# Kernel tuning notes

Measured on AMD Instinct MI355X. Metric: run time of the kernel, lower is better.

The kernel has to match this reference:

```python
import jax, jax.numpy as jnp
import numpy as np

N_CLASSES = 10   # number of distinct private-attribute labels
DIM = 16         # PCA / GMM dimension (init arg `dim`)
SIGMA = 1.0      # init arg `sigma`, cov = sigma * I


def _pca(X, k):
    # torch PCA: center, SVD of X^T, project onto first k left singular vectors
    X = X - jnp.mean(X, axis=0)
    U, _, _ = jnp.linalg.svd(X.T, full_matrices=False)  # U: [D, min(D,B)]
    return X @ U[:, :k]                                  # [B, k]


def _gmm_loss(x, labels):
    # x: [B, k] PCA-projected features, labels: [B] int class ids in [0, C)
    B = x.shape[0]
    dtype = x.dtype
    ones = jnp.ones((B,), dtype)
    counts = jax.ops.segment_sum(ones, labels, num_segments=N_CLASSES)          # [C]
    sums = jax.ops.segment_sum(x, labels, num_segments=N_CLASSES)               # [C, k]
    safe = jnp.maximum(counts, 1.0)
    means = sums / safe[:, None]                                                # [C, k]

    diff = x - means[labels]                                                    # [B, k]
    outers = diff[:, :, None] * diff[:, None, :]                                # [B, k, k]
    Ssum = jax.ops.segment_sum(outers, labels, num_segments=N_CLASSES)          # [C, k, k]
    Sigma = SIGMA * jnp.eye(DIM, dtype=dtype) + Ssum / safe[:, None, None]      # [C, k, k]

    inv = jnp.linalg.inv(Sigma)                                                 # [C, k, k]
    _, logdet = jnp.linalg.slogdet(Sigma)                                       # [C]

    # KL(N_i || N_j) = 0.5*(tr(S_j^-1 S_i) + (u_j-u_i)^T S_j^-1 (u_j-u_i) - k + logdet_j - logdet_i)
    tr = jnp.einsum('jab,iba->ij', inv, Sigma)                                  # [C, C]
    d = means[None, :, :] - means[:, None, :]                                   # d[i,j] = u_j - u_i
    maha = jnp.einsum('ija,jab,ijb->ij', d, inv, d)                             # [C, C]
    kl = 0.5 * (tr + maha - DIM + logdet[None, :] - logdet[:, None])            # [C, C]

    present = counts > 0
    W = counts[:, None] * counts[None, :]
    mask = present[:, None] & present[None, :] & ~jnp.eye(N_CLASSES, dtype=bool)
    result = jnp.sum(jnp.where(mask, kl * W, jnp.zeros_like(kl)))
    return result / (jnp.asarray(B, dtype) ** 3)


def setup_inputs() -> dict:
    key = jax.random.key(0)
    k1, k2 = jax.random.split(key)
    mu = jax.random.normal(k1, (16384, 1024), dtype=jnp.float32)
    private_attribute = jax.random.randint(k2, (16384,), 0, N_CLASSES, dtype=jnp.int32)
    return {"mu": mu, "private_attribute": private_attribute}


def reference(mu, private_attribute):
    B = mu.shape[0]
    x = mu.reshape(B, -1)          # flatten(start_dim=1)
    x = _pca(x, DIM)               # [B, DIM]
    labels = private_attribute.astype(jnp.int32)
    return _gmm_loss(x, labels)
```

## Files before the change

kernel.cpp:

```cpp
#include <hip/hip_runtime.h>
#include <math.h>

#define BN 16384
#define DN 1024

static constexpr size_t OFF_C    = 0x000000;
static constexpr size_t OFF_P    = 0x400000;
static constexpr size_t OFF_Y0   = 0x800000;
static constexpr size_t OFF_Y1   = 0x840000;
static constexpr size_t OFF_Y2   = 0x880000;
static constexpr size_t OFF_Y3   = 0x8C0000;
static constexpr size_t OFF_CQ   = 0x900000;
static constexpr size_t OFF_S64  = 0x940000;
static constexpr size_t OFF_LF   = 0x948000;
static constexpr size_t OFF_T64  = 0x950000;
static constexpr size_t OFF_V16  = 0x958000;
static constexpr size_t OFF_UT   = 0x960000;
static constexpr size_t OFF_UTT  = 0x970000;
static constexpr size_t OFF_S16  = 0x980000;
static constexpr size_t OFF_CS   = 0x980100;
static constexpr size_t OFF_TR   = 0x981100;
static constexpr size_t OFF_SCAL = 0x981200;
static constexpr size_t OFF_STAT = 0x981300;
static constexpr size_t OFF_F    = 0x990000;
static constexpr size_t OFF_M    = 0xA90000;

typedef float f32x4 __attribute__((ext_vector_type(4)));
typedef short bf16x8 __attribute__((ext_vector_type(8)));
typedef unsigned int u32x4v __attribute__((ext_vector_type(4)));

__device__ __forceinline__ float wsumf(float v){
  #pragma unroll
  for (int off=32; off; off>>=1) v += __shfl_xor(v, off, 64);
  return v;
}
__device__ __forceinline__ float wminf(float v){
  #pragma unroll
  for (int off=32; off; off>>=1) v = fminf(v, __shfl_xor(v, off, 64));
  return v;
}
__device__ __forceinline__ float wmaxf(float v){
  #pragma unroll
  for (int off=32; off; off>>=1) v = fmaxf(v, __shfl_xor(v, off, 64));
  return v;
}
__device__ __forceinline__ float lanebc(float x, int l){
  return __int_as_float(__builtin_amdgcn_readlane(__float_as_int(x), l));
}
__device__ __forceinline__ float wred64(float x){
  x += __int_as_float(__builtin_amdgcn_update_dpp(0, __float_as_int(x), 0x118, 0xf, 0xf, true));
  x += __int_as_float(__builtin_amdgcn_update_dpp(0, __float_as_int(x), 0x114, 0xf, 0xf, true));
  x += __int_as_float(__builtin_amdgcn_update_dpp(0, __float_as_int(x), 0x112, 0xf, 0xf, true));
  x += __int_as_float(__builtin_amdgcn_update_dpp(0, __float_as_int(x), 0x111, 0xf, 0xf, true));
  float s0 = lanebc(x, 15), s1 = lanebc(x, 31), s2 = lanebc(x, 47), s3 = lanebc(x, 63);
  return (s0 + s1) + (s2 + s3);
}


__global__ __launch_bounds__(256) void colsum_k(const float* __restrict__ X, float* __restrict__ cs){
  int b = blockIdx.x, t = threadIdx.x;
  float a0=0.f,a1=0.f,a2=0.f,a3=0.f;
  for (int r=0; r<64; ++r){
    const float4 v = *(const float4*)(X + (size_t)(b*64 + r)*1024 + t*4);
    a0 += v.x; a1 += v.y; a2 += v.z; a3 += v.w;
  }
  atomicAdd(&cs[t*4+0], a0); atomicAdd(&cs[t*4+1], a1);
  atomicAdd(&cs[t*4+2], a2); atomicAdd(&cs[t*4+3], a3);
}

#define SYRK_SLICES 27
#define SYRK_KCHUNK 608
#define SYRKM_SLICES 4
#define SYRKM_KCHUNK 256

__device__ __forceinline__ f32x4 mfma32(bf16x8 a, bf16x8 b, f32x4 c){
  return __builtin_amdgcn_mfma_f32_16x16x32_bf16(a, b, c, 0, 0, 0);
}

__device__ __forceinline__ int lds_woff(int c, int chunk){
  return c*20 + (((chunk ^ ((c>>3)&3)) & 3) << 2);
}

template<int KCHUNK>
__device__ __forceinline__ void syrk_mfma_body(const float* __restrict__ X, float* __restrict__ G, int KMAX){
  int bx = blockIdx.x;
  int tp = bx % 36, ks = bx / 36;
  int ti = 0, rem = tp;
  while (rem >= 8 - ti){ rem -= 8 - ti; ++ti; }
  int tj = ti + rem;
  int k0 = ks * KCHUNK;
  int kend = k0 + KCHUNK; if (kend > KMAX) kend = KMAX;

  __shared__ __attribute__((aligned(16))) unsigned int LdsT[2][3][128][20];

  int t = threadIdx.x;
  int wid = t >> 6, lane = t & 63;
  int wr = wid >> 1, wc = wid & 1;
  int lm = lane & 15;
  int lk = lane >> 4;

  f32x4 acc[4][4];
  #pragma unroll
  for (int i=0;i<4;++i)
    #pragma unroll
    for (int j=0;j<4;++j) acc[i][j] = (f32x4){0.f,0.f,0.f,0.f};

  for (int kc = k0; kc < kend; kc += 32){
    __syncthreads();
    #pragma unroll
    for (int w=0; w<4; ++w){
      int job = t + 256*w;
      int c   = job & 127;
      int pk  = job >> 7;
      int p   = pk >> 2;
      int kpg = pk & 3;
      const float* src = X + (size_t)(kc + kpg*8)*1024 + (p ? tj : ti)*128 + c;
      float e[8];
      #pragma unroll
      for (int i=0;i<8;++i) e[i] = src[(size_t)i*1024];
      unsigned hh[8]; float r2f[8]; unsigned mm[8];
      #pragma unroll
      for (int i=0;i<8;++i){
        unsigned u = __float_as_uint(e[i]);
        hh[i] = u & 0xFFFF0000u;
        float r1 = e[i] - __uint_as_float(hh[i]);
        mm[i] = __float_as_uint(r1) & 0xFFFF0000u;
        r2f[i] = r1 - __uint_as_float(mm[i]);
      }
      u32x4v hp, mp, lp;
      #pragma unroll
      for (int j=0;j<4;++j){
        hp[j] = (hh[2*j] >> 16) | hh[2*j+1];
        mp[j] = (mm[2*j] >> 16) | mm[2*j+1];
        lp[j] = (__float_as_uint(r2f[2*j]) >> 16) | (__float_as_uint(r2f[2*j+1]) & 0xFFFF0000u);
      }
      int wo = lds_woff(c, kpg);
      *(u32x4v*)(&LdsT[p][0][0][0] + wo) = hp;
      *(u32x4v*)(&LdsT[p][1][0][0] + wo) = mp;
      *(u32x4v*)(&LdsT[p][2][0][0] + wo) = lp;
    }
    __syncthreads();
    bf16x8 af[3][4], bg[3][4];
    #pragma unroll
    for (int fm=0; fm<4; ++fm){
      int ca = wr*64 + fm*16 + lm;
      int cb = wc*64 + fm*16 + lm;
      int woa = lds_woff(ca, lk);
      int wob = lds_woff(cb, lk);
      #pragma unroll
      for (int tm=0; tm<3; ++tm){
        af[tm][fm] = *(const bf16x8*)(&LdsT[0][tm][0][0] + woa);
        bg[tm][fm] = *(const bf16x8*)(&LdsT[1][tm][0][0] + wob);
      }
    }
    #pragma unroll
    for (int fm=0; fm<4; ++fm)
      #pragma unroll
      for (int fn=0; fn<4; ++fn){
        f32x4 a = acc[fm][fn];
        a = mfma32(af[0][fm], bg[0][fn], a);
        a = mfma32(af[0][fm], bg[1][fn], a);
        a = mfma32(af[1][fm], bg[0][fn], a);
        a = mfma32(af[0][fm], bg[2][fn], a);
        a = mfma32(af[2][fm], bg[0][fn], a);
        a = mfma32(af[1][fm], bg[1][fn], a);
        acc[fm][fn] = a;
      }
  }
  #pragma unroll
  for (int fm=0; fm<4; ++fm){
    int gi = ti*128 + wr*64 + fm*16 + lk*4;
    #pragma unroll
    for (int fn=0; fn<4; ++fn){
      int gj = tj*128 + wc*64 + fn*16 + lm;
      #pragma unroll
      for (int rg=0; rg<4; ++rg)
        atomicAdd(&G[(size_t)(gi+rg)*1024 + gj], acc[fm][fn][rg]);
    }
  }
}

__global__ __launch_bounds__(256, 2) void syrk_mfma_k(const float* __restrict__ X, float* __restrict__ G){
  syrk_mfma_body<SYRK_KCHUNK>(X, G, 16384);
}
__global__ __launch_bounds__(256, 2) void syrkM_mfma_k(const float* __restrict__ X, float* __restrict__ G){
  syrk_mfma_body<SYRKM_KCHUNK>(X, G, 1024);
}

__global__ __launch_bounds__(256) void trace_k(const float* __restrict__ G, const float* __restrict__ cs,
                                               float* __restrict__ scal){
  __shared__ float red[4];
  int t = threadIdx.x;
  float s = 0.f;
  #pragma unroll
  for (int w=0; w<4; ++w){
    int i = t + 256*w;
    float d = cs[i];
    s += G[(size_t)i*1025] - d*d*(1.0f/16384.0f);
  }
  s = wsumf(s);
  if ((t & 63) == 0) red[t >> 6] = s;
  __syncthreads();
  if (t == 0){
    float trD = (red[0]+red[1]+red[2]+red[3]) * (1.0f/1024.0f);
    float c = 1.40f * trD, a = 0.25f * trD;
    scal[0] = 0.5f*(c + a);
    scal[1] = 2.0f/(c - a);
  }
}

__global__ __launch_bounds__(256) void formCChat_k(float* __restrict__ C, const float* __restrict__ cs,
                                                   const float* __restrict__ scal){
  int g = blockIdx.x*256 + threadIdx.x;
  int i = g >> 10, j = g & 1023;
  if (j < i) return;
  float mid = scal[0], ie = scal[1];
  float v = C[g] - cs[i]*cs[j]*(1.0f/16384.0f);
  float h = ie*(v - ((i==j) ? mid : 0.f));
  C[g] = h;
  C[j*1024 + i] = h;
}

__global__ __launch_bounds__(256) void formM_k(float* __restrict__ M){
  int g = blockIdx.x*256 + threadIdx.x;
  int i = g >> 10, j = g & 1023;
  if (j < i) return;
  float v = 2.f*M[g] - ((i==j) ? 1.f : 0.f);
  M[g] = v;
  M[j*1024 + i] = v;
}

__global__ void rng_k(float* __restrict__ Y){
  int idx = blockIdx.x*256 + threadIdx.x;
  unsigned h = (unsigned)idx * 2654435761u;
  h ^= h >> 16; h *= 2246822519u; h ^= h >> 13; h *= 3266489917u; h ^= h >> 16;
  Y[idx] = (float)(h & 0xFFFFFFu) * (2.0f/16777216.0f) - 1.0f;
}

__global__ __launch_bounds__(256) void mv_k(const float* __restrict__ Yt, const float* __restrict__ Cm, float* __restrict__ P){
  int bx = blockIdx.x;
  int nt = bx & 15, ks = bx >> 4;
  int n0 = nt*64, k0 = ks*64;
  __shared__ __attribute__((aligned(16))) float At[64][68];
  __shared__ __attribute__((aligned(16))) float Bt[64][68];
  int t = threadIdx.x;
  #pragma unroll
  for (int w=0; w<4; ++w){
    int job = t + 256*w;
    int m  = job >> 4, f4 = job & 15;
    float4 v = *(const float4*)(Yt + (size_t)m*1024 + k0 + f4*4);
    At[f4*4+0][m] = v.x; At[f4*4+1][m] = v.y; At[f4*4+2][m] = v.z; At[f4*4+3][m] = v.w;
    int kk = job >> 4, fn = job & 15;
    *(float4*)&Bt[kk][fn*4] = *(const float4*)(Cm + (size_t)(k0+kk)*1024 + n0 + fn*4);
  }
  __syncthreads();
  int tm = t & 15, tn = t >> 4;
  float acc[4][4];
  #pragma unroll
  for (int i=0;i<4;++i)
    #pragma unroll
    for (int j=0;j<4;++j) acc[i][j]=0.f;
  for (int kk=0; kk<64; ++kk){
    float4 a = *(const float4*)&At[kk][tm*4];
    float4 b = *(const float4*)&Bt[kk][tn*4];
    float av[4] = {a.x,a.y,a.z,a.w};
    float bv[4] = {b.x,b.y,b.z,b.w};
    #pragma unroll
    for (int i=0;i<4;++i)
      #pragma unroll
      for (int j=0;j<4;++j) acc[i][j] += av[i]*bv[j];
  }
  #pragma unroll
  for (int i=0;i<4;++i){
    float4 o; o.x=acc[i][0]; o.y=acc[i][1]; o.z=acc[i][2]; o.w=acc[i][3];
    *(float4*)(P + (size_t)(ks*64 + tm*4 + i)*1024 + n0 + tn*4) = o;
  }
}

__global__ __launch_bounds__(256) void combine_k(const float* __restrict__ P, const float* __restrict__ Tk1,
                                                 float* __restrict__ out, int mode){
  int idx = (blockIdx.x*256 + threadIdx.x)*4;
  float s0=0.f,s1=0.f,s2=0.f,s3=0.f;
  #pragma unroll
  for (int ks=0; ks<16; ++ks){
    const float4 p = *(const float4*)(P + (size_t)ks*65536 + idx);
    s0 += p.x; s1 += p.y; s2 += p.z; s3 += p.w;
  }
  float4 o;
  if (mode == 0){
    o.x=s0; o.y=s1; o.z=s2; o.w=s3;
  } else {
    const float4 t1 = *(const float4*)(Tk1 + idx);
    o.x = 2.f*s0 - t1.x; o.y = 2.f*s1 - t1.y;
    o.z = 2.f*s2 - t1.z; o.w = 2.f*s3 - t1.w;
  }
  *(float4*)(out+idx) = o;
}

__global__ __launch_bounds__(256) void gram_k(const float* __restrict__ A, const float* __restrict__ Bm, double* __restrict__ S){
  int bx = blockIdx.x;
  int i = bx >> 2, jg = bx & 3;
  __shared__ __attribute__((aligned(16))) float Ai[1024];
  __shared__ double red[16][17];
  int t = threadIdx.x;
  ((float4*)Ai)[t] = ((const float4*)(A + (size_t)i*1024))[t];
  __syncthreads();
  int jl = t >> 4, kp = t & 15;
  const float* Br = Bm + (size_t)(jg*16 + jl)*1024 + kp*64;
  const float* Ar = Ai + kp*64;
  double acc = 0.0;
  #pragma unroll 8
  for (int kk=0; kk<64; ++kk) acc += (double)Br[kk] * (double)Ar[kk];
  red[jl][kp] = acc;
  __syncthreads();
  if (t < 16){
    double s = 0.0;
    #pragma unroll
    for (int p2=0; p2<16; ++p2) s += red[t][p2];
    S[i*64 + jg*16 + t] = s;
  }
}

__global__ __launch_bounds__(64) void chol_k(const double* __restrict__ S, float* __restrict__ Lf){
  __shared__ double L[64][65];
  __shared__ double col[64];
  int t = threadIdx.x;
  for (int e=t; e<4096; e+=64) L[e>>6][e&63] = S[e];
  __syncthreads();
  for (int k=0; k<64; ++k){
    double lkk = sqrt(fmax(L[k][k], 1e-280));
    double r = 1.0/lkk;
    double ck = (t > k) ? L[t][k]*r : 0.0;
    col[t] = ck;
    if (t == k) L[k][k] = lkk;
    if (t > k)  L[t][k] = ck;
    __syncthreads();
    #pragma unroll
    for (int j=0; j<64; j+=8){
      L[t][j+0] -= ck*col[j+0];
      L[t][j+1] -= ck*col[j+1];
      L[t][j+2] -= ck*col[j+2];
      L[t][j+3] -= ck*col[j+3];
      L[t][j+4] -= ck*col[j+4];
      L[t][j+5] -= ck*col[j+5];
      L[t][j+6] -= ck*col[j+6];
      L[t][j+7] -= ck*col[j+7];
    }
    __syncthreads();
  }
  for (int e=t; e<4096; e+=64){
    int i = e >> 6, j = e & 63;
    Lf[e] = (j < i) ? (float)L[i][j] : ((j == i) ? (float)(1.0/L[i][i]) : 0.f);
  }
}

__global__ __launch_bounds__(256) void applysolve_k(const float* __restrict__ Yin, const float* __restrict__ Lf, float* __restrict__ Qout){
  int k = blockIdx.x*256 + threadIdx.x;
  float z[64];
  #pragma unroll
  for (int c=0; c<64; ++c){
    float v = Yin[(size_t)c*1024 + k];
    #pragma unroll
    for (int j=0; j<c; ++j) v -= Lf[c*64+j]*z[j];
    z[c] = v * Lf[c*64+c];
  }
  #pragma unroll
  for (int c=0; c<64; ++c) Qout[(size_t)c*1024 + k] = z[c];
}

__global__ __launch_bounds__(256) void eig16_k(const double* __restrict__ Tin, float* __restrict__ V16){
  __shared__ float A[64][65];
  __shared__ float dF[64], eF[64], e2F[64], kapS[64];
  __shared__ float lamF[16];
  __shared__ float IV[5][64][16];
  __shared__ float W[16][68];
  int t = threadIdx.x;
  int r = t & 63, p4 = t >> 6;

  for (int e=t; e<4096; e+=256){
    int i = e >> 6, j = e & 63;
    A[i][j] = (float)(0.5*(Tin[i*64+j] + Tin[(size_t)j*64+i]));
  }
  __syncthreads();

  if (p4 == 0){
    float a[64];
    #pragma unroll
    for (int j=0; j<64; ++j) a[j] = A[r][j];
    float ck = a[0];
    #pragma unroll 1
    for (int k=0; k<62; ++k){
      int kp1 = k + 1;
      int jb0 = k >> 4;
      bool below = (r > k);
      float ckm = below ? ck : 0.f;
      float sig = wred64(ckm*ckm);
      float x1 = lanebc(ck, kp1);
      float rr = sqrtf(sig);
      float alpha = (x1 >= 0.f) ? -rr : rr;
      float kappa = sig - alpha*x1;
      float kinv = (kappa > 1e-30f) ? 1.f/kappa : 0.f;
      float v = ckm;
      if (r == kp1) v = x1 - alpha;
      if (kinv == 0.f) v = 0.f;
      if (r == 0){ eF[k] = (kinv==0.f) ? 0.f : alpha; kapS[k] = (kinv==0.f) ? 0.f : kappa; }
      if (r == k) dF[k] = ck;
      if (below) A[r][k] = v;
      float pf = 0.f;
      #pragma unroll
      for (int jb=0; jb<4; ++jb){
        if (jb >= jb0){
          #pragma unroll
          for (int jj=0; jj<16; ++jj){
            int j = jb*16 + jj;
            pf += a[j]*lanebc(v, j);
          }
        }
      }
      float pi = below ? pf*kinv : 0.f;
      float vp = wred64(v*pi);
      float Kc = vp*0.5f*kinv;
      float q = below ? (pi - Kc*v) : 0.f;
      float ckn = 0.f;
      #pragma unroll
      for (int jb=0; jb<4; ++jb){
        if (jb >= jb0){
          #pragma unroll
          for (int jj=0; jj<16; ++jj){
            int j = jb*16 + jj;
            float vj = lanebc(v, j);
            float qj = lanebc(q, j);
            float an = a[j] - (v*qj + q*vj);
            a[j] = an;
            ckn = (j == kp1) ? an : ckn;
          }
        }
      }
      ck = ckn;
    }
    if (r == 62) dF[62] = ck;
    if (r == 63){ eF[62] = ck; dF[63] = a[63]; }
    if (r == 0){ eF[63] = 0.f; kapS[62] = 0.f; kapS[63] = 0.f; }
  }
  __syncthreads();
  if (t < 64) e2F[t] = eF[t]*eF[t];
  __syncthreads();

  float em1 = (r > 0) ? fabsf(eF[r-1]) : 0.f;
  float ep  = fabsf(eF[r]);
  float glo = wminf(dF[r] - em1 - ep);
  float ghi = wmaxf(dF[r] + em1 + ep);
  float span = ghi - glo + 1.f;
  float lo = glo - 0.001f*span, hi = ghi + 0.001f*span;

  int eidx = t >> 4, g = t & 15;
  int m = 48 + eidx;
  for (int it=0; it<7; ++it){
    float x = lo + (hi - lo)*((float)(g+1)*(1.0f/17.0f));
    float qq = dF[0] - x;
    int c = (qq < 0.f) ? 1 : 0;
    #pragma unroll
    for (int j=1; j<64; ++j){
      float aq = fabsf(qq);
      float qs = (aq < 1e-10f) ? ((qq < 0.f) ? -1e-10f : 1e-10f) : qq;
      qq = dF[j] - x - e2F[j-1]*__builtin_amdgcn_rcpf(qs);
      c += (qq < 0.f) ? 1 : 0;
    }
    float cl = (c <= m) ? x : -3.4e38f;
    float ch = (c >  m) ? x :  3.4e38f;
    #pragma unroll
    for (int off=1; off<16; off<<=1){
      cl = fmaxf(cl, __shfl_xor(cl, off, 64));
      ch = fminf(ch, __shfl_xor(ch, off, 64));
    }
    lo = fmaxf(lo, cl);
    hi = fminf(hi, ch);
  }
  if (g == 0) lamF[eidx] = 0.5f*(lo + hi);
  __syncthreads();

  if (t < 16){
    float lam = lamF[t];
    const float PIVF = 1e-6f;
    #pragma unroll 4
    for (int i=0; i<64; ++i){
      unsigned hsh = (unsigned)(i*131 + t*1009 + 7);
      hsh ^= hsh >> 13; hsh *= 2654435761u; hsh ^= hsh >> 16;
      IV[4][i][t] = (float)(hsh & 0xFFFF) * (1.5f/65536.0f) + 0.25f;
    }
    unsigned long long piv = 0ull;
    float dcur = dF[0] - lam;
    float ducur = eF[0];
    for (int i=0; i<63; ++i){
      float dli = eF[i];
      float dnext = dF[i+1] - lam;
      float eip1 = (i < 62) ? eF[i+1] : 0.f;
      bool sw = fabsf(dcur) < fabsf(dli);
      float dd = dcur;
      if (fabsf(dd) < PIVF) dd = (dd < 0.f) ? -PIVF : PIVF;
      float f = sw ? (dcur*__builtin_amdgcn_rcpf(dli)) : (dli*__builtin_amdgcn_rcpf(dd));
      float ddst = sw ? dli : dd;
      float dust = sw ? dnext : ducur;
      float du2  = sw ? eip1 : 0.f;
      float dnew = sw ? (ducur - f*dnext) : (dnext - f*ducur);
      float dunew= sw ? (-f*eip1) : eip1;
      if (sw) piv |= (1ull << i);
      IV[0][i][t] = f;
      float dc = ddst; if (fabsf(dc) < PIVF) dc = (dc < 0.f) ? -PIVF : PIVF;
      IV[1][i][t] = __builtin_amdgcn_rcpf(dc);
      IV[2][i][t] = dust;
      IV[3][i][t] = du2;
      dcur = dnew; ducur = dunew;
    }
    { float dc = dcur; if (fabsf(dc) < PIVF) dc = (dc < 0.f) ? -PIVF : PIVF; IV[1][63][t] = __builtin_amdgcn_rcpf(dc); }
    float ss = 0.f;
    #pragma unroll 1
    for (int iter=0; iter<2; ++iter){
      float scale = (iter == 0) ? 1.f : rsqrtf(fmaxf(ss, 1e-30f));
      float b = IV[4][0][t]*scale;
      #pragma unroll 7
      for (int i=0; i<63; ++i){
        float bn = IV[4][i+1][t]*scale;
        float f = IV[0][i][t];
        bool sw = (piv >> i) & 1ull;
        float keep = sw ? bn : b;
        float bnew = (sw ? b : bn) - f*keep;
        IV[4][i][t] = keep;
        b = bnew;
      }
      ss = 0.f;
      float x1v = b * IV[1][63][t];
      IV[4][63][t] = x1v; ss += x1v*x1v;
      float x0v = (IV[4][62][t] - IV[2][62][t]*x1v) * IV[1][62][t];
      IV[4][62][t] = x0v; ss += x0v*x0v;
      float xp1 = x0v, xp2 = x1v;
      #pragma unroll 7
      for (int i=61; i>=0; --i){
        float xi = (IV[4][i][t] - IV[2][i][t]*xp1 - IV[3][i][t]*xp2) * IV[1][i][t];
        IV[4][i][t] = xi; ss += xi*xi;
        xp2 = xp1; xp1 = xi;
      }
    }
    #pragma unroll 4
    for (int i=0; i<64; ++i) W[t][i] = IV[4][i][t];
  }
  __syncthreads();

  for (int c=0; c<16; ++c){
    float wi = (t < 64) ? W[c][t] : 0.f;
    float s2 = wred64(wi*wi);
    float rn = rsqrtf(fmaxf(s2, 1e-30f));
    wi *= rn;
    if (t < 64) W[c][t] = wi;
    __syncthreads();
    for (int c2=c+1; c2<16; ++c2){
      float w2 = (t < 64) ? W[c2][t] : 0.f;
      float d2 = wred64(wi*w2);
      if (t < 64) W[c2][t] -= d2*wi;
    }
    __syncthreads();
  }

  int cL = (p4 << 2) + (r >> 4);
  int part = r & 15;
  for (int k=61; k>=0; --k){
    float kpd = kapS[k];
    if (kpd == 0.f) continue;
    float invk = 1.f/kpd;
    float vv[4];
    float ps = 0.f;
    #pragma unroll
    for (int mm=0; mm<4; ++mm){
      int i = part*4 + mm;
      vv[mm] = (i > k) ? A[i][k] : 0.f;
      ps += vv[mm]*W[cL][i];
    }
    ps += __shfl_xor(ps, 1, 64);
    ps += __shfl_xor(ps, 2, 64);
    ps += __shfl_xor(ps, 4, 64);
    ps += __shfl_xor(ps, 8, 64);
    float sc = ps * invk;
    #pragma unroll
    for (int mm=0; mm<4; ++mm){
      int i = part*4 + mm;
      W[cL][i] -= vv[mm]*sc;
    }
  }
  __syncthreads();

  for (int e=t; e<1024; e+=256){
    int j = e >> 4, c = e & 15;
    V16[e] = W[c][j];
  }
}

__global__ __launch_bounds__(256) void buildUt_k(const float* __restrict__ V16,
                                                 const float* __restrict__ Qt, float* __restrict__ Ut, float* __restrict__ UtT){
  int bx = blockIdx.x;
  int c = bx & 15, kc = bx >> 4;
  int k = kc*256 + threadIdx.x;
  float acc = 0.f;
  #pragma unroll
  for (int j=0; j<64; ++j) acc += V16[j*16 + c] * Qt[(size_t)j*1024 + k];
  Ut[(size_t)c*1024 + k] = acc;
  UtT[(size_t)k*16 + c] = acc;
}

__global__ void s16_k(const float* __restrict__ cs, const float* __restrict__ Ut, float* __restrict__ s16){
  __shared__ float red[16][17];
  int t = threadIdx.x;
  int c = t & 15, part = t >> 4;
  float acc = 0.f;
  for (int d=0; d<64; ++d) acc += cs[part*64 + d] * Ut[(size_t)c*1024 + part*64 + d];
  red[c][part] = acc;
  __syncthreads();
  if (t < 16){
    float s = 0.f;
    #pragma unroll
    for (int p2=0; p2<16; ++p2) s += red[t][p2];
    s16[t] = s * (1.0f/16384.0f);
  }
}

__global__ __launch_bounds__(256) void proj_k(const float* __restrict__ X, const float* __restrict__ UtT,
                                              const float* __restrict__ s16, float* __restrict__ F){
  int r0 = blockIdx.x * 64;
  int t = threadIdx.x;
  __shared__ __attribute__((aligned(16))) float uts[16384];
  #pragma unroll
  for (int w=0; w<16; ++w)
    ((float4*)uts)[t + 256*w] = ((const float4*)UtT)[t + 256*w];
  __syncthreads();
  int row = t & 63, kp = t >> 6;
  const float* xr = X + (size_t)(r0 + row)*1024 + kp*256;
  const float* ut = uts + kp*256*16;
  float acc[16];
  #pragma unroll
  for (int c=0;c<16;++c) acc[c] = 0.f;
  for (int dd=0; dd<256; dd+=4){
    float4 xv4 = *(const float4*)(xr + dd);
    float xv[4] = {xv4.x, xv4.y, xv4.z, xv4.w};
    #pragma unroll
    for (int u=0; u<4; ++u)
      #pragma unroll
      for (int c=0;c<16;++c) acc[c] += xv[u] * ut[(dd+u)*16 + c];
  }
  __shared__ float part[4][64][16];
  #pragma unroll
  for (int c=0;c<16;++c) part[kp][row][c] = acc[c];
  __syncthreads();
  int cq = t >> 6;
  #pragma unroll
  for (int ccx=0; ccx<4; ++ccx){
    int c = cq*4 + ccx;
    float v = part[0][row][c] + part[1][row][c] + part[2][row][c] + part[3][row][c] - s16[c];
    F[(size_t)(r0 + row)*16 + c] = v;
  }
}

__global__ __launch_bounds__(256) void stats_k(const float* __restrict__ F, const int* __restrict__ lbl, float* __restrict__ SG){
  __shared__ float st[10][154];
  int t = threadIdx.x;
  for (int e=t; e<1540; e+=256) st[e/154][e%154] = 0.f;
  __syncthreads();
  int r = blockIdx.x*256 + t;
  float f[16];
  #pragma unroll
  for (int w=0; w<4; ++w){
    float4 v = *(const float4*)(F + (size_t)r*16 + w*4);
    f[w*4+0]=v.x; f[w*4+1]=v.y; f[w*4+2]=v.z; f[w*4+3]=v.w;
  }
  int c = lbl[r];
  if ((unsigned)c < 10u){
    float* bs = &st[c][0];
    atomicAdd(&bs[0], 1.f);
    #pragma unroll
    for (int a=0;a<16;++a) atomicAdd(&bs[1+a], f[a]);
    int sidx = 17;
    #pragma unroll
    for (int a=0;a<16;++a)
      #pragma unroll
      for (int b2=a;b2<16;++b2) atomicAdd(&bs[sidx++], f[a]*f[b2]);
  }
  __syncthreads();
  for (int e=t; e<1530; e+=256) atomicAdd(&SG[e], st[e/153][e%153]);
}

__global__ __launch_bounds__(256) void final_k(const float* __restrict__ SG, float* __restrict__ out){
  __shared__ double cnt[10], safe[10], ldet[10];
  __shared__ double mean[10][16];
  __shared__ double Sig[10][16][16];
  __shared__ double Inv[10][16][16];
  __shared__ double red[128];
  int t = threadIdx.x;
  if (t < 10){
    double c0 = (double)SG[t*153];
    cnt[t] = c0; safe[t] = (c0 > 0.0) ? c0 : 1.0;
  }
  __syncthreads();
  for (int e=t; e<160; e+=256){
    int c = e >> 4, a = e & 15;
    mean[c][a] = (double)SG[c*153 + 1 + a] / safe[c];
  }
  __syncthreads();
  for (int e=t; e<2560; e+=256){
    int c = e >> 8, ab = e & 255, a = ab >> 4, b2 = ab & 15;
    int lo = a < b2 ? a : b2, hi = a < b2 ? b2 : a;
    int ti = lo*(33 - lo)/2 + (hi - lo);
    Sig[c][a][b2] = (double)SG[c*153 + 17 + ti]/safe[c] - mean[c][a]*mean[c][b2] + ((a==b2)?1.0:0.0);
  }
  __syncthreads();
  if (t < 10){
    for (int a=0;a<16;++a)
      for (int b2=0;b2<16;++b2) Inv[t][a][b2] = Sig[t][a][b2];
    double ld2 = 0.0;
    for (int k=0;k<16;++k){
      double v = Inv[t][k][k];
      for (int j=0;j<k;++j) v -= Inv[t][k][j]*Inv[t][k][j];
      v = fmax(v, 1e-280);
      double lkk = sqrt(v);
      Inv[t][k][k] = lkk; ld2 += log(lkk);
      for (int i=k+1;i<16;++i){
        double w = Inv[t][i][k];
        for (int j=0;j<k;++j) w -= Inv[t][i][j]*Inv[t][k][j];
        Inv[t][i][k] = w / lkk;
      }
    }
    ldet[t] = 2.0*ld2;
    for (int j=0;j<16;++j){
      double dj = 1.0 / Inv[t][j][j];
      Inv[t][j][j] = dj;
      for (int i=j+1;i<16;++i){
        double ssum = Inv[t][i][j]*dj;
        for (int k=j+1;k<i;++k) ssum += Inv[t][i][k]*Inv[t][k][j];
        Inv[t][i][j] = -ssum / Inv[t][i][i];
      }
    }
    double dg[16];
    #pragma unroll
    for (int a=0;a<16;++a){
      double s2 = 0.0;
      for (int k=a;k<16;++k){ double x = Inv[t][k][a]; s2 += x*x; }
      dg[a] = s2;
    }
    for (int a=0;a<16;++a)
      for (int b2=a+1;b2<16;++b2){
        double s2 = 0.0;
        for (int k=b2;k<16;++k) s2 += Inv[t][k][a]*Inv[t][k][b2];
        Inv[t][a][b2] = s2;
      }
    for (int a=0;a<16;++a) Inv[t][a][a] = dg[a];
    for (int a=0;a<16;++a)
      for (int b2=a+1;b2<16;++b2) Inv[t][b2][a] = Inv[t][a][b2];
  }
  __syncthreads();
  double contrib = 0.0;
  if (t < 100){
    int i = t/10, j = t%10;
    if (i != j && cnt[i] > 0.0 && cnt[j] > 0.0){
      double tr = 0.0;
      for (int a=0;a<16;++a)
        for (int b2=0;b2<16;++b2) tr += Inv[j][a][b2]*Sig[i][b2][a];
      double dm[16];
      #pragma unroll
      for (int a=0;a<16;++a) dm[a] = mean[j][a] - mean[i][a];
      double mah = 0.0;
      for (int a=0;a<16;++a){
        double rs = 0.0;
        for (int b2=0;b2<16;++b2) rs += Inv[j][a][b2]*dm[b2];
        mah += dm[a]*rs;
      }
      double kl = 0.5*(tr + mah - 16.0 + ldet[j] - ldet[i]);
      contrib = kl * cnt[i]*cnt[j];
    }
  }
  if (t < 128) red[t] = contrib;
  __syncthreads();
  for (int off=64; off>0; off >>= 1){
    if (t < off) red[t] += red[t+off];
    __syncthreads();
  }
  if (t == 0) out[0] = (float)(red[0] / (16384.0*16384.0*16384.0));
}

extern "C" void kernel_launch(void* const* d_in, const int* in_sizes, int n_in,
                              void* d_out, int out_size, void* d_ws, size_t ws_size,
                              hipStream_t stream){
  (void)in_sizes; (void)n_in; (void)out_size; (void)ws_size;
  const float* X  = (const float*)d_in[0];
  const int* lbl  = (const int*)d_in[1];
  char* ws = (char*)d_ws;
  float*  C    = (float*)(ws + OFF_C);
  float*  Mm   = (float*)(ws + OFF_M);
  float*  P    = (float*)(ws + OFF_P);
  float*  Y0   = (float*)(ws + OFF_Y0);
  float*  Y1   = (float*)(ws + OFF_Y1);
  float*  Y2   = (float*)(ws + OFF_Y2);
  float*  Y3   = (float*)(ws + OFF_Y3);
  float*  CQ   = (float*)(ws + OFF_CQ);
  double* S64  = (double*)(ws + OFF_S64);
  float*  LF   = (float*)(ws + OFF_LF);
  double* T64  = (double*)(ws + OFF_T64);
  float*  V16  = (float*)(ws + OFF_V16);
  float*  UT   = (float*)(ws + OFF_UT);
  float*  UTT  = (float*)(ws + OFF_UTT);
  float*  S16  = (float*)(ws + OFF_S16);
  float*  CS   = (float*)(ws + OFF_CS);
  float*  SCAL = (float*)(ws + OFF_SCAL);
  float*  STAT = (float*)(ws + OFF_STAT);
  float*  F    = (float*)(ws + OFF_F);
  float*  OUT  = (float*)d_out;

  hipMemsetAsync(C, 0, 4*1024*1024, stream);
  hipMemsetAsync(Mm, 0, 4*1024*1024, stream);
  hipMemsetAsync(ws + OFF_CS, 0, 12800, stream);

  colsum_k<<<256, 256, 0, stream>>>(X, CS);
  syrk_mfma_k<<<36*SYRK_SLICES, 256, 0, stream>>>(X, C);
  trace_k<<<1, 256, 0, stream>>>(C, CS, SCAL);
  formCChat_k<<<4096, 256, 0, stream>>>(C, CS, SCAL);
  syrkM_mfma_k<<<36*SYRKM_SLICES, 256, 0, stream>>>(C, Mm);
  formM_k<<<4096, 256, 0, stream>>>(Mm);
  hipMemsetAsync(P, 0, 4*1024*1024, stream);
  syrkM_mfma_k<<<36*SYRKM_SLICES, 256, 0, stream>>>(Mm, P);
  formM_k<<<4096, 256, 0, stream>>>(P);
  hipMemsetAsync(C, 0, 4*1024*1024, stream);
  syrkM_mfma_k<<<36*SYRKM_SLICES, 256, 0, stream>>>(P, C);
  formM_k<<<4096, 256, 0, stream>>>(C);
  rng_k<<<256, 256, 0, stream>>>(Y0);

  auto cheb2 = [&](float* U, float* Wb, float* Ob){
    mv_k<<<256, 256, 0, stream>>>(U, C, P);
    combine_k<<<64, 256, 0, stream>>>(P, U, Wb, 0);
    mv_k<<<256, 256, 0, stream>>>(Wb, C, P);
    combine_k<<<64, 256, 0, stream>>>(P, U, Ob, 1);
  };
  auto cholqr = [&](float* Yin, float* Qout){
    gram_k<<<256, 256, 0, stream>>>(Yin, Yin, S64);
    chol_k<<<1, 64, 0, stream>>>(S64, LF);
    applysolve_k<<<4, 256, 0, stream>>>(Yin, LF, Qout);
  };

  cheb2(Y0, Y1, Y2);
  cholqr(Y2, Y0);
  cheb2(Y0, Y1, Y2);
  cholqr(Y2, Y1);
  cholqr(Y1, Y3);

  mv_k<<<256, 256, 0, stream>>>(Y3, Mm, P);
  combine_k<<<64, 256, 0, stream>>>(P, Y3, CQ, 0);
  gram_k<<<256, 256, 0, stream>>>(Y3, CQ, T64);
  eig16_k<<<1, 256, 0, stream>>>(T64, V16);
  buildUt_k<<<64, 256, 0, stream>>>(V16, Y3, UT, UTT);

  s16_k<<<1, 256, 0, stream>>>(CS, UT, S16);
  proj_k<<<256, 256, 0, stream>>>(X, UTT, S16, F);
  stats_k<<<64, 256, 0, stream>>>(F, lbl, STAT);
  final_k<<<1, 256, 0, stream>>>(STAT, OUT);
}
```

Before: 1.129 ms.

## Fuse Chebyshev squaring epilogues, drop third bf16 split term, merge Cholesky with solve

The matrix-squaring SYRK calls now run as one k-slice per output tile, so each block owns its whole tile. The 2*M - I transform and symmetric mirror are written straight from registers, which removes the memsets, atomics and separate formM_k passes. Every SYRK also drops from a three-term to a two-term bf16 split, cutting MFMA work by a third at some cost in precision. The Cholesky factor and triangular solve are fused into one 1024-thread block, but now run on a single CU instead of four blocks.

```diff
diff --git a/kernel.cpp b/kernel.cpp
--- a/kernel.cpp
+++ b/kernel.cpp
@@ -70,8 +70,6 @@
 
 #define SYRK_SLICES 27
 #define SYRK_KCHUNK 608
-#define SYRKM_SLICES 4
-#define SYRKM_KCHUNK 256
 
 __device__ __forceinline__ f32x4 mfma32(bf16x8 a, bf16x8 b, f32x4 c){
   return __builtin_amdgcn_mfma_f32_16x16x32_bf16(a, b, c, 0, 0, 0);
@@ -81,7 +79,7 @@
   return c*20 + (((chunk ^ ((c>>3)&3)) & 3) << 2);
 }
 
-template<int KCHUNK>
+template<int KCHUNK, int T2MODE>
 __device__ __forceinline__ void syrk_mfma_body(const float* __restrict__ X, float* __restrict__ G, int KMAX){
   int bx = blockIdx.x;
   int tp = bx % 36, ks = bx / 36;
@@ -91,7 +89,7 @@
   int k0 = ks * KCHUNK;
   int kend = k0 + KCHUNK; if (kend > KMAX) kend = KMAX;
 
-  __shared__ __attribute__((aligned(16))) unsigned int LdsT[2][3][128][20];
+  __shared__ __attribute__((aligned(16))) unsigned int LdsT[2][2][128][20];
 
   int t = threadIdx.x;
   int wid = t >> 6, lane = t & 63;
@@ -118,29 +116,26 @@
       float e[8];
       #pragma unroll
       for (int i=0;i<8;++i) e[i] = src[(size_t)i*1024];
-      unsigned hh[8]; float r2f[8]; unsigned mm[8];
+      unsigned hh[8], mm[8];
       #pragma unroll
       for (int i=0;i<8;++i){
         unsigned u = __float_as_uint(e[i]);
         hh[i] = u & 0xFFFF0000u;
         float r1 = e[i] - __uint_as_float(hh[i]);
         mm[i] = __float_as_uint(r1) & 0xFFFF0000u;
-        r2f[i] = r1 - __uint_as_float(mm[i]);
-      }
-      u32x4v hp, mp, lp;
+      }
+      u32x4v hp, mp;
       #pragma unroll
       for (int j=0;j<4;++j){
         hp[j] = (hh[2*j] >> 16) | hh[2*j+1];
         mp[j] = (mm[2*j] >> 16) | mm[2*j+1];
-        lp[j] = (__float_as_uint(r2f[2*j]) >> 16) | (__float_as_uint(r2f[2*j+1]) & 0xFFFF0000u);
       }
       int wo = lds_woff(c, kpg);
       *(u32x4v*)(&LdsT[p][0][0][0] + wo) = hp;
       *(u32x4v*)(&LdsT[p][1][0][0] + wo) = mp;
-      *(u32x4v*)(&LdsT[p][2][0][0] + wo) = lp;
     }
     __syncthreads();
-    bf16x8 af[3][4], bg[3][4];
+    bf16x8 af[2][4], bg[2][4];
     #pragma unroll
     for (int fm=0; fm<4; ++fm){
       int ca = wr*64 + fm*16 + lm;
@@ -148,7 +143,7 @@
       int woa = lds_woff(ca, lk);
       int wob = lds_woff(cb, lk);
       #pragma unroll
-      for (int tm=0; tm<3; ++tm){
+      for (int tm=0; tm<2; ++tm){
         af[tm][fm] = *(const bf16x8*)(&LdsT[0][tm][0][0] + woa);
         bg[tm][fm] = *(const bf16x8*)(&LdsT[1][tm][0][0] + wob);
       }
@@ -161,8 +156,6 @@
         a = mfma32(af[0][fm], bg[0][fn], a);
         a = mfma32(af[0][fm], bg[1][fn], a);
         a = mfma32(af[1][fm], bg[0][fn], a);
-        a = mfma32(af[0][fm], bg[2][fn], a);
-        a = mfma32(af[2][fm], bg[0][fn], a);
         a = mfma32(af[1][fm], bg[1][fn], a);
         acc[fm][fn] = a;
       }
@@ -174,17 +167,25 @@
     for (int fn=0; fn<4; ++fn){
       int gj = tj*128 + wc*64 + fn*16 + lm;
       #pragma unroll
-      for (int rg=0; rg<4; ++rg)
-        atomicAdd(&G[(size_t)(gi+rg)*1024 + gj], acc[fm][fn][rg]);
+      for (int rg=0; rg<4; ++rg){
+        if (T2MODE){
+          int gii = gi + rg;
+          float v = 2.f*acc[fm][fn][rg] - ((gii==gj) ? 1.f : 0.f);
+          G[(size_t)gii*1024 + gj] = v;
+          G[(size_t)gj*1024 + gii] = v;
+        } else {
+          atomicAdd(&G[(size_t)(gi+rg)*1024 + gj], acc[fm][fn][rg]);
+        }
+      }
     }
   }
 }
 
 __global__ __launch_bounds__(256, 2) void syrk_mfma_k(const float* __restrict__ X, float* __restrict__ G){
-  syrk_mfma_body<SYRK_KCHUNK>(X, G, 16384);
-}
-__global__ __launch_bounds__(256, 2) void syrkM_mfma_k(const float* __restrict__ X, float* __restrict__ G){
-  syrk_mfma_body<SYRKM_KCHUNK>(X, G, 1024);
+  syrk_mfma_body<SYRK_KCHUNK, 0>(X, G, 16384);
+}
+__global__ __launch_bounds__(256, 2) void syrkT2_k(const float* __restrict__ X, float* __restrict__ G){
+  syrk_mfma_body<1024, 1>(X, G, 1024);
 }
 
 __global__ __launch_bounds__(256) void trace_k(const float* __restrict__ G, const float* __restrict__ cs,
@@ -221,15 +222,6 @@
   C[j*1024 + i] = h;
 }
 
-__global__ __launch_bounds__(256) void formM_k(float* __restrict__ M){
-  int g = blockIdx.x*256 + threadIdx.x;
-  int i = g >> 10, j = g & 1023;
-  if (j < i) return;
-  float v = 2.f*M[g] - ((i==j) ? 1.f : 0.f);
-  M[g] = v;
-  M[j*1024 + i] = v;
-}
-
 __global__ void rng_k(float* __restrict__ Y){
   int idx = blockIdx.x*256 + threadIdx.x;
   unsigned h = (unsigned)idx * 2654435761u;
@@ -321,51 +313,50 @@
   }
 }
 
-__global__ __launch_bounds__(64) void chol_k(const double* __restrict__ S, float* __restrict__ Lf){
+__global__ __launch_bounds__(1024) void cholsolve_k(const double* __restrict__ S,
+                                                    const float* __restrict__ Yin, float* __restrict__ Qout){
   __shared__ double L[64][65];
-  __shared__ double col[64];
-  int t = threadIdx.x;
-  for (int e=t; e<4096; e+=64) L[e>>6][e&63] = S[e];
-  __syncthreads();
-  for (int k=0; k<64; ++k){
-    double lkk = sqrt(fmax(L[k][k], 1e-280));
-    double r = 1.0/lkk;
-    double ck = (t > k) ? L[t][k]*r : 0.0;
-    col[t] = ck;
-    if (t == k) L[k][k] = lkk;
-    if (t > k)  L[t][k] = ck;
-    __syncthreads();
-    #pragma unroll
-    for (int j=0; j<64; j+=8){
-      L[t][j+0] -= ck*col[j+0];
-      L[t][j+1] -= ck*col[j+1];
-      L[t][j+2] -= ck*col[j+2];
-      L[t][j+3] -= ck*col[j+3];
-      L[t][j+4] -= ck*col[j+4];
-      L[t][j+5] -= ck*col[j+5];
-      L[t][j+6] -= ck*col[j+6];
-      L[t][j+7] -= ck*col[j+7];
-    }
-    __syncthreads();
-  }
-  for (int e=t; e<4096; e+=64){
-    int i = e >> 6, j = e & 63;
-    Lf[e] = (j < i) ? (float)L[i][j] : ((j == i) ? (float)(1.0/L[i][i]) : 0.f);
-  }
-}
-
-__global__ __launch_bounds__(256) void applysolve_k(const float* __restrict__ Yin, const float* __restrict__ Lf, float* __restrict__ Qout){
-  int k = blockIdx.x*256 + threadIdx.x;
+  __shared__ double colD[64];
+  __shared__ float LfS[64][65];
+  int t = threadIdx.x;
+  for (int e=t; e<4096; e+=1024) L[e>>6][e&63] = S[e];
+  __syncthreads();
+  if (t < 64){
+    for (int k=0; k<64; ++k){
+      double lkk = sqrt(fmax(L[k][k], 1e-280));
+      double r = 1.0/lkk;
+      double ck = (t > k) ? L[t][k]*r : 0.0;
+      colD[t] = ck;
+      if (t == k) L[k][k] = lkk;
+      if (t > k)  L[t][k] = ck;
+      #pragma unroll
+      for (int j=0; j<64; j+=8){
+        L[t][j+0] -= ck*colD[j+0];
+        L[t][j+1] -= ck*colD[j+1];
+        L[t][j+2] -= ck*colD[j+2];
+        L[t][j+3] -= ck*colD[j+3];
+        L[t][j+4] -= ck*colD[j+4];
+        L[t][j+5] -= ck*colD[j+5];
+        L[t][j+6] -= ck*colD[j+6];
+        L[t][j+7] -= ck*colD[j+7];
+      }
+    }
+    for (int e=t; e<4096; e+=64){
+      int i = e >> 6, j = e & 63;
+      LfS[i][j] = (j < i) ? (float)L[i][j] : ((j == i) ? (float)(1.0/L[i][i]) : 0.f);
+    }
+  }
+  __syncthreads();
   float z[64];
   #pragma unroll
   for (int c=0; c<64; ++c){
-    float v = Yin[(size_t)c*1024 + k];
-    #pragma unroll
-    for (int j=0; j<c; ++j) v -= Lf[c*64+j]*z[j];
-    z[c] = v * Lf[c*64+c];
-  }
-  #pragma unroll
-  for (int c=0; c<64; ++c) Qout[(size_t)c*1024 + k] = z[c];
+    float v = Yin[(size_t)c*1024 + t];
+    #pragma unroll
+    for (int j=0; j<c; ++j) v -= LfS[c][j]*z[j];
+    z[c] = v * LfS[c][c];
+  }
+  #pragma unroll
+  for (int c=0; c<64; ++c) Qout[(size_t)c*1024 + t] = z[c];
 }
 
 __global__ __launch_bounds__(256) void eig16_k(const double* __restrict__ Tin, float* __restrict__ V16){
@@ -799,7 +790,6 @@
   float*  Y3   = (float*)(ws + OFF_Y3);
   float*  CQ   = (float*)(ws + OFF_CQ);
   double* S64  = (double*)(ws + OFF_S64);
-  float*  LF   = (float*)(ws + OFF_LF);
   double* T64  = (double*)(ws + OFF_T64);
   float*  V16  = (float*)(ws + OFF_V16);
   float*  UT   = (float*)(ws + OFF_UT);
@@ -812,21 +802,15 @@
   float*  OUT  = (float*)d_out;
 
   hipMemsetAsync(C, 0, 4*1024*1024, stream);
-  hipMemsetAsync(Mm, 0, 4*1024*1024, stream);
   hipMemsetAsync(ws + OFF_CS, 0, 12800, stream);
 
   colsum_k<<<256, 256, 0, stream>>>(X, CS);
   syrk_mfma_k<<<36*SYRK_SLICES, 256, 0, stream>>>(X, C);
   trace_k<<<1, 256, 0, stream>>>(C, CS, SCAL);
   formCChat_k<<<4096, 256, 0, stream>>>(C, CS, SCAL);
-  syrkM_mfma_k<<<36*SYRKM_SLICES, 256, 0, stream>>>(C, Mm);
-  formM_k<<<4096, 256, 0, stream>>>(Mm);
-  hipMemsetAsync(P, 0, 4*1024*1024, stream);
-  syrkM_mfma_k<<<36*SYRKM_SLICES, 256, 0, stream>>>(Mm, P);
-  formM_k<<<4096, 256, 0, stream>>>(P);
-  hipMemsetAsync(C, 0, 4*1024*1024, stream);
-  syrkM_mfma_k<<<36*SYRKM_SLICES, 256, 0, stream>>>(P, C);
-  formM_k<<<4096, 256, 0, stream>>>(C);
+  syrkT2_k<<<36, 256, 0, stream>>>(C, Mm);
+  syrkT2_k<<<36, 256, 0, stream>>>(Mm, P);
+  syrkT2_k<<<36, 256, 0, stream>>>(P, C);
   rng_k<<<256, 256, 0, stream>>>(Y0);
 
   auto cheb2 = [&](float* U, float* Wb, float* Ob){
@@ -837,8 +821,7 @@
   };
   auto cholqr = [&](float* Yin, float* Qout){
     gram_k<<<256, 256, 0, stream>>>(Yin, Yin, S64);
-    chol_k<<<1, 64, 0, stream>>>(S64, LF);
-    applysolve_k<<<4, 256, 0, stream>>>(Yin, LF, Qout);
+    cholsolve_k<<<1, 1024, 0, stream>>>(S64, Yin, Qout);
   };
 
   cheb2(Y0, Y1, Y2);
```

Measured after the change: 1.126 ms. About the same (-0.3%).
